# Optimization experiments

Hardware: AMD Instinct MI355X
Metric: run time of the kernel (lower is better)

Reference implementation:

```python
import jax, jax.numpy as jnp
import numpy as np

R, S, C, HID = 8192, 128, 32, 64   # rays, samples/ray, grid_chn, mlp_hidden_chn
G = 128                            # voxel grid resolution
COLOR_CHN = 3
NUM_HARM = 3
OPACITY_INIT_BIAS = -5.0
GAIN = 1.0
HE_DIM = 3 * 2 * NUM_HARM + 3      # harmonic embedding dim = 21

def _relu(x):
    return jnp.maximum(x, 0.0)

def _trilinear(grid, p):
    # grid: [G, G, G, Cg] indexed [z, y, x]; p: [N, 3] xyz coords in [-1, 1]
    g = grid.shape[0]
    c = (p + 1.0) * 0.5 * (g - 1)  # align_corners=True convention
    c0f = jnp.floor(c)
    fr = c - c0f
    c0 = jnp.clip(c0f.astype(jnp.int32), 0, g - 1)
    c1 = jnp.clip(c0 + 1, 0, g - 1)
    x0, y0, z0 = c0[:, 0], c0[:, 1], c0[:, 2]
    x1, y1, z1 = c1[:, 0], c1[:, 1], c1[:, 2]
    fx, fy, fz = fr[:, 0:1], fr[:, 1:2], fr[:, 2:3]
    out = jnp.zeros((p.shape[0], grid.shape[-1]), grid.dtype)
    for xi, wx in ((x0, 1.0 - fx), (x1, fx)):
        for yi, wy in ((y0, 1.0 - fy), (y1, fy)):
            for zi, wz in ((z0, 1.0 - fz), (z1, fz)):
                out = out + (wx * wy * wz) * grid[zi, yi, xi]
    return out

def _harmonic(d):
    # [sin(2^i d), cos(2^i d)] for i<NUM_HARM, with raw direction appended
    freqs = 2.0 ** jnp.arange(NUM_HARM, dtype=jnp.float32)
    ang = d[:, None, :] * freqs[None, :, None]  # [R, NH, 3]
    n = d.shape[0]
    return jnp.concatenate([jnp.sin(ang).reshape(n, -1), jnp.cos(ang).reshape(n, -1), d], axis=-1)

def _forward(origins, directions, near, far, feature_grid, Wr, br, Wt1, bt1, Wt2, bt2, Wo1, bo1, Wo2, bo2, Wc1, bc1, Wc2, bc2):
    n_rays = origins.shape[0]
    # stratified midpoints between near and far
    t = near[:, None] + (far - near)[:, None] * (jnp.arange(S, dtype=jnp.float32) + 0.5) / S
    pts = origins[:, None, :] + t[..., None] * directions[:, None, :]  # [R, S, 3]
    feats = _trilinear(feature_grid, pts.reshape(-1, 3)).reshape(n_rays, S, -1)
    # trunk MLP
    e = _relu(feats @ Wt1 + bt1)
    e = _relu(e @ Wt2 + bt2)
    # opacity MLP (last-layer bias carries opacity_init_bias)
    raw = _relu(e @ Wo1 + bo1) @ Wo2 + bo2  # [R, S, 1]
    density = jax.nn.softplus(GAIN * raw[..., 0])
    delta = ((far - near) / S)[:, None]
    alpha = 1.0 - jnp.exp(-delta * density)  # [R, S]
    trans = jnp.cumprod(1.0 - alpha, axis=1)
    T = jnp.concatenate([jnp.ones((n_rays, 1), alpha.dtype), trans[:, :-1]], axis=1)
    w = T * alpha  # compositing weights
    # color branch: harmonic ray-direction encoding added to color-MLP input
    ray_enc = _harmonic(directions) @ Wr + br  # [R, HID]
    cin = e + ray_enc[:, None, :]
    col = jax.nn.sigmoid(_relu(cin @ Wc1 + bc1) @ Wc2 + bc2)  # [R, S, COLOR_CHN]
    color = jnp.einsum('rs,rsc->rc', w, col)
    mask = 1.0 - trans[:, -1]
    color = color + (1.0 - mask)[:, None] * 0.0  # bg_color = 0.0
    return color, mask

def setup_inputs():
    key = jax.random.key(0)
    ks = jax.random.split(key, 16)
    directions = jax.random.normal(ks[0], (R, 3), jnp.float32)
    directions = directions / jnp.linalg.norm(directions, axis=-1, keepdims=True)
    origins = jnp.zeros((R, 3), jnp.float32)
    near = jnp.full((R,), 0.1, jnp.float32)
    far = jnp.full((R,), 1.0, jnp.float32)
    feature_grid = jax.random.normal(ks[1], (G, G, G, C), jnp.float32) * 0.1
    def lin(k, i, o):
        s = (2.0 / (i + o)) ** 0.5
        return jax.random.normal(k, (i, o), jnp.float32) * s
    return {
        'origins': origins, 'directions': directions, 'near': near, 'far': far,
        'feature_grid': feature_grid,
        'Wr': lin(ks[2], HE_DIM, HID), 'br': jnp.zeros((HID,), jnp.float32),
        'Wt1': lin(ks[3], C, HID), 'bt1': jnp.zeros((HID,), jnp.float32),
        'Wt2': lin(ks[4], HID, HID), 'bt2': jnp.zeros((HID,), jnp.float32),
        'Wo1': lin(ks[5], HID, HID), 'bo1': jnp.zeros((HID,), jnp.float32),
        'Wo2': lin(ks[6], HID, 1), 'bo2': jnp.full((1,), OPACITY_INIT_BIAS, jnp.float32),
        'Wc1': lin(ks[7], HID, HID), 'bc1': jnp.zeros((HID,), jnp.float32),
        'Wc2': lin(ks[8], HID, COLOR_CHN), 'bc2': jnp.zeros((COLOR_CHN,), jnp.float32),
    }

def reference(origins, directions, near, far, feature_grid, Wr, br, Wt1, bt1, Wt2, bt2, Wo1, bo1, Wo2, bo2, Wc1, bc1, Wc2, bc2):
    return _forward(origins, directions, near, far, feature_grid, Wr, br, Wt1, bt1, Wt2, bt2, Wo1, bo1, Wo2, bo2, Wc1, bc1, Wc2, bc2)
```

## Files before the change

### kernel.cpp

```cpp
#include <hip/hip_runtime.h>
#include <math.h>

#define NRAYS 8192
#define XPAD 72

typedef short s16x8 __attribute__((ext_vector_type(8)));
typedef float f32x4 __attribute__((ext_vector_type(4)));

__device__ __forceinline__ unsigned short f2bf(float x){
  unsigned u = __float_as_uint(x);
  u += 0x7FFF + ((u >> 16) & 1);
  return (unsigned short)(u >> 16);
}
__device__ __forceinline__ float bf2f(unsigned short s){ return __uint_as_float(((unsigned)s) << 16); }
__device__ __forceinline__ float softplusf_(float x){ return (x > 20.f) ? x : log1pf(expf(x)); }
__device__ __forceinline__ float sigmoidf_(float x){ return 1.f / (1.f + expf(-x)); }

__global__ void prep_weights(const float* __restrict__ Wt1, const float* __restrict__ Wt2,
                             const float* __restrict__ Wo1, const float* __restrict__ Wc1,
                             unsigned short* __restrict__ ws)
{
  const int i0 = blockIdx.x * blockDim.x + threadIdx.x;
  const int st = gridDim.x * blockDim.x;
  for (int i = i0; i < 2048; i += st){ int n = i >> 5, k = i & 31; ws[i]         = f2bf(Wt1[k * 64 + n]); }
  for (int i = i0; i < 4096; i += st){ int n = i >> 6, k = i & 63; ws[2048 + i]  = f2bf(Wt2[k * 64 + n]); }
  for (int i = i0; i < 4096; i += st){ int n = i >> 6, k = i & 63; ws[6144 + i]  = f2bf(Wo1[k * 64 + n]); }
  for (int i = i0; i < 4096; i += st){ int n = i >> 6, k = i & 63; ws[10240 + i] = f2bf(Wc1[k * 64 + n]); }
}

__device__ __forceinline__ void layer64(const s16x8 a[4][2], const unsigned short* __restrict__ wt,
                                        const float* __restrict__ bias, int ln15, int quad,
                                        f32x4 acc[4][4])
{
  float bv[4];
#pragma unroll
  for (int nt = 0; nt < 4; ++nt) bv[nt] = bias[nt * 16 + ln15];
#pragma unroll
  for (int mt = 0; mt < 4; ++mt)
#pragma unroll
    for (int nt = 0; nt < 4; ++nt){ f32x4 c; c[0] = bv[nt]; c[1] = bv[nt]; c[2] = bv[nt]; c[3] = bv[nt]; acc[mt][nt] = c; }
#pragma unroll
  for (int ks = 0; ks < 2; ++ks){
    s16x8 b[4];
#pragma unroll
    for (int nt = 0; nt < 4; ++nt)
      b[nt] = *(const s16x8*)(wt + (nt * 16 + ln15) * 64 + ks * 32 + quad * 8);
#pragma unroll
    for (int mt = 0; mt < 4; ++mt)
#pragma unroll
      for (int nt = 0; nt < 4; ++nt)
        acc[mt][nt] = __builtin_amdgcn_mfma_f32_16x16x32_bf16(a[mt][ks], b[nt], acc[mt][nt], 0, 0, 0);
  }
}

__device__ __forceinline__ void store_relu(unsigned short* __restrict__ sX, int wrow, int ln15, int quad,
                                           const f32x4 acc[4][4])
{
#pragma unroll
  for (int mt = 0; mt < 4; ++mt){
    const int rowb = wrow + mt * 16 + quad * 4;
#pragma unroll
    for (int nt = 0; nt < 4; ++nt){
      const int col = nt * 16 + ln15;
#pragma unroll
      for (int r = 0; r < 4; ++r)
        sX[(rowb + r) * XPAD + col] = f2bf(fmaxf(acc[mt][nt][r], 0.f));
    }
  }
}

extern "C" __global__ __launch_bounds__(256, 2)
void lightplane_fwd(const float* __restrict__ origins, const float* __restrict__ dirs,
                    const float* __restrict__ nearv,   const float* __restrict__ farv,
                    const float* __restrict__ grid,
                    const float* __restrict__ Wr,  const float* __restrict__ br,
                    const float* __restrict__ bt1, const float* __restrict__ bt2,
                    const float* __restrict__ bo1,
                    const float* __restrict__ Wo2, const float* __restrict__ bo2,
                    const float* __restrict__ bc1,
                    const float* __restrict__ Wc2, const float* __restrict__ bc2,
                    const unsigned short* __restrict__ ws,
                    float* __restrict__ out)
{
  __shared__ unsigned short s_X[256 * XPAD];
  __shared__ float s_scan[2][128];
  __shared__ float s_enc[2][64];
  __shared__ float s_part[2][2][4];

  const int tid   = threadIdx.x;
  const int lane  = tid & 63;
  const int wv    = tid >> 6;
  const int ln15  = lane & 15, quad = lane >> 4;
  const int wrow  = wv * 64;
  const int r_loc = tid >> 7;
  const int s_idx = tid & 127;
  const int ray   = blockIdx.x * 2 + r_loc;

  if (tid < 128) {
    const int rr = tid >> 6, j = tid & 63;
    const int rg = blockIdx.x * 2 + rr;
    const float ddx = dirs[rg * 3 + 0], ddy = dirs[rg * 3 + 1], ddz = dirs[rg * 3 + 2];
    float h[21]; float f = 1.f;
#pragma unroll
    for (int q = 0; q < 3; ++q) {
      h[q * 3 + 0] = sinf(ddx * f); h[q * 3 + 1] = sinf(ddy * f); h[q * 3 + 2] = sinf(ddz * f);
      h[9 + q * 3 + 0] = cosf(ddx * f); h[9 + q * 3 + 1] = cosf(ddy * f); h[9 + q * 3 + 2] = cosf(ddz * f);
      f *= 2.f;
    }
    h[18] = ddx; h[19] = ddy; h[20] = ddz;
    float a = br[j];
#pragma unroll
    for (int i = 0; i < 21; ++i) a = fmaf(h[i], Wr[i * 64 + j], a);
    s_enc[rr][j] = a;
  }

  const float dx = dirs[ray * 3 + 0], dy = dirs[ray * 3 + 1], dz = dirs[ray * 3 + 2];
  const float ox = origins[ray * 3 + 0], oy = origins[ray * 3 + 1], oz = origins[ray * 3 + 2];
  const float nr = nearv[ray], fa = farv[ray];
  const float t  = nr + (fa - nr) * ((s_idx + 0.5f) * (1.0f / 128.0f));
  const float px = fmaf(t, dx, ox), py = fmaf(t, dy, oy), pz = fmaf(t, dz, oz);

  const float cx = (px + 1.f) * 63.5f, cy = (py + 1.f) * 63.5f, cz = (pz + 1.f) * 63.5f;
  const float fx0 = floorf(cx), fy0 = floorf(cy), fz0 = floorf(cz);
  const float frx = cx - fx0, fry = cy - fy0, frz = cz - fz0;
  int ix0 = min(max((int)fx0, 0), 127), iy0 = min(max((int)fy0, 0), 127), iz0 = min(max((int)fz0, 0), 127);
  int ix1 = min(ix0 + 1, 127), iy1 = min(iy0 + 1, 127), iz1 = min(iz0 + 1, 127);
  const float wxs[2] = {1.f - frx, frx}, wys[2] = {1.f - fry, fry}, wzs[2] = {1.f - frz, frz};
  const int xi[2] = {ix0, ix1}, yi[2] = {iy0, iy1}, zi[2] = {iz0, iz1};

  float fe[32];
#pragma unroll
  for (int k = 0; k < 32; ++k) fe[k] = 0.f;
#pragma unroll
  for (int a = 0; a < 2; ++a)
#pragma unroll
    for (int b2 = 0; b2 < 2; ++b2)
#pragma unroll
      for (int c2 = 0; c2 < 2; ++c2) {
        const float wgt = wzs[a] * wys[b2] * wxs[c2];
        const float4* g4 = (const float4*)(grid + ((size_t)((zi[a] * 128 + yi[b2]) * 128 + xi[c2])) * 32);
#pragma unroll
        for (int k = 0; k < 8; ++k) {
          float4 g = g4[k];
          fe[4 * k + 0] = fmaf(wgt, g.x, fe[4 * k + 0]);
          fe[4 * k + 1] = fmaf(wgt, g.y, fe[4 * k + 1]);
          fe[4 * k + 2] = fmaf(wgt, g.z, fe[4 * k + 2]);
          fe[4 * k + 3] = fmaf(wgt, g.w, fe[4 * k + 3]);
        }
      }

#pragma unroll
  for (int q = 0; q < 4; ++q) {
    s16x8 v;
#pragma unroll
    for (int j = 0; j < 8; ++j) v[j] = (short)f2bf(fe[q * 8 + j]);
    *(s16x8*)&s_X[tid * XPAD + q * 8] = v;
  }

  f32x4 acc[4][4];

  {
    s16x8 a1[4];
#pragma unroll
    for (int mt = 0; mt < 4; ++mt)
      a1[mt] = *(const s16x8*)&s_X[(wrow + mt * 16 + ln15) * XPAD + quad * 8];
    float bv[4];
#pragma unroll
    for (int nt = 0; nt < 4; ++nt) bv[nt] = bt1[nt * 16 + ln15];
#pragma unroll
    for (int mt = 0; mt < 4; ++mt)
#pragma unroll
      for (int nt = 0; nt < 4; ++nt){ f32x4 c; c[0]=bv[nt];c[1]=bv[nt];c[2]=bv[nt];c[3]=bv[nt]; acc[mt][nt]=c; }
    s16x8 b[4];
#pragma unroll
    for (int nt = 0; nt < 4; ++nt)
      b[nt] = *(const s16x8*)(ws + (nt * 16 + ln15) * 32 + quad * 8);
#pragma unroll
    for (int mt = 0; mt < 4; ++mt)
#pragma unroll
      for (int nt = 0; nt < 4; ++nt)
        acc[mt][nt] = __builtin_amdgcn_mfma_f32_16x16x32_bf16(a1[mt], b[nt], acc[mt][nt], 0, 0, 0);
    store_relu(s_X, wrow, ln15, quad, acc);
  }

  {
    s16x8 a[4][2];
#pragma unroll
    for (int ks = 0; ks < 2; ++ks)
#pragma unroll
      for (int mt = 0; mt < 4; ++mt)
        a[mt][ks] = *(const s16x8*)&s_X[(wrow + mt * 16 + ln15) * XPAD + ks * 32 + quad * 8];
    layer64(a, ws + 2048, bt2, ln15, quad, acc);
    store_relu(s_X, wrow, ln15, quad, acc);
  }

  s16x8 ea[4][2];
#pragma unroll
  for (int ks = 0; ks < 2; ++ks)
#pragma unroll
    for (int mt = 0; mt < 4; ++mt)
      ea[mt][ks] = *(const s16x8*)&s_X[(wrow + mt * 16 + ln15) * XPAD + ks * 32 + quad * 8];

  layer64(ea, ws + 6144, bo1, ln15, quad, acc);
  store_relu(s_X, wrow, ln15, quad, acc);
  float raw = bo2[0];
#pragma unroll
  for (int q = 0; q < 8; ++q) {
    s16x8 v = *(const s16x8*)&s_X[tid * XPAD + q * 8];
#pragma unroll
    for (int j = 0; j < 8; ++j)
      raw = fmaf(bf2f((unsigned short)v[j]), Wo2[q * 8 + j], raw);
  }
  const float density = softplusf_(raw);
  const float delta   = (fa - nr) * (1.0f / 128.0f);
  const float alpha   = 1.f - expf(-delta * density);

  __syncthreads();

  {
    s16x8 a[4][2];
#pragma unroll
    for (int ks = 0; ks < 2; ++ks) {
      const float* ep = &s_enc[r_loc][ks * 32 + quad * 8];
      float4 e0 = *(const float4*)ep;
      float4 e1 = *(const float4*)(ep + 4);
      float encv[8] = {e0.x, e0.y, e0.z, e0.w, e1.x, e1.y, e1.z, e1.w};
#pragma unroll
      for (int mt = 0; mt < 4; ++mt) {
        s16x8 v;
#pragma unroll
        for (int j = 0; j < 8; ++j)
          v[j] = (short)f2bf(bf2f((unsigned short)ea[mt][ks][j]) + encv[j]);
        a[mt][ks] = v;
      }
    }
    layer64(a, ws + 10240, bc1, ln15, quad, acc);
    store_relu(s_X, wrow, ln15, quad, acc);
  }
  float c0 = bc2[0], c1 = bc2[1], c2 = bc2[2];
#pragma unroll
  for (int q = 0; q < 8; ++q) {
    s16x8 v = *(const s16x8*)&s_X[tid * XPAD + q * 8];
#pragma unroll
    for (int j = 0; j < 8; ++j) {
      const float h = bf2f((unsigned short)v[j]);
      c0 = fmaf(h, Wc2[(q * 8 + j) * 3 + 0], c0);
      c1 = fmaf(h, Wc2[(q * 8 + j) * 3 + 1], c1);
      c2 = fmaf(h, Wc2[(q * 8 + j) * 3 + 2], c2);
    }
  }
  c0 = sigmoidf_(c0); c1 = sigmoidf_(c1); c2 = sigmoidf_(c2);

  float vv = 1.f - alpha;
  s_scan[r_loc][s_idx] = vv;
  __syncthreads();
#pragma unroll
  for (int off = 1; off < 128; off <<= 1) {
    const float u = (s_idx >= off) ? s_scan[r_loc][s_idx - off] : 1.f;
    __syncthreads();
    vv *= u;
    s_scan[r_loc][s_idx] = vv;
    __syncthreads();
  }
  const float Texcl = (s_idx == 0) ? 1.f : s_scan[r_loc][s_idx - 1];
  const float wgt = Texcl * alpha;

  float p0 = wgt * c0, p1 = wgt * c1, p2 = wgt * c2;
#pragma unroll
  for (int off = 32; off > 0; off >>= 1) {
    p0 += __shfl_down(p0, off, 64);
    p1 += __shfl_down(p1, off, 64);
    p2 += __shfl_down(p2, off, 64);
  }
  if ((tid & 63) == 0) {
    const int wvi = s_idx >> 6;
    s_part[r_loc][wvi][0] = p0; s_part[r_loc][wvi][1] = p1; s_part[r_loc][wvi][2] = p2;
  }
  __syncthreads();
  if (s_idx == 0) {
    out[ray * 3 + 0] = s_part[r_loc][0][0] + s_part[r_loc][1][0];
    out[ray * 3 + 1] = s_part[r_loc][0][1] + s_part[r_loc][1][1];
    out[ray * 3 + 2] = s_part[r_loc][0][2] + s_part[r_loc][1][2];
    out[NRAYS * 3 + ray] = 1.f - s_scan[r_loc][127];
  }
}

extern "C" void kernel_launch(void* const* d_in, const int* in_sizes, int n_in,
                              void* d_out, int out_size, void* d_ws, size_t ws_size,
                              hipStream_t stream)
{
  (void)in_sizes; (void)n_in; (void)out_size; (void)ws_size;
  const float* origins = (const float*)d_in[0];
  const float* dirs    = (const float*)d_in[1];
  const float* nearv   = (const float*)d_in[2];
  const float* farv    = (const float*)d_in[3];
  const float* grid    = (const float*)d_in[4];
  const float* Wr  = (const float*)d_in[5];
  const float* br  = (const float*)d_in[6];
  const float* Wt1 = (const float*)d_in[7];
  const float* bt1 = (const float*)d_in[8];
  const float* Wt2 = (const float*)d_in[9];
  const float* bt2 = (const float*)d_in[10];
  const float* Wo1 = (const float*)d_in[11];
  const float* bo1 = (const float*)d_in[12];
  const float* Wo2 = (const float*)d_in[13];
  const float* bo2 = (const float*)d_in[14];
  const float* Wc1 = (const float*)d_in[15];
  const float* bc1 = (const float*)d_in[16];
  const float* Wc2 = (const float*)d_in[17];
  const float* bc2 = (const float*)d_in[18];
  unsigned short* ws = (unsigned short*)d_ws;
  float* out = (float*)d_out;

  prep_weights<<<16, 256, 0, stream>>>(Wt1, Wt2, Wo1, Wc1, ws);
  lightplane_fwd<<<NRAYS / 2, 256, 0, stream>>>(origins, dirs, nearv, farv, grid,
                                                Wr, br, bt1, bt2, bo1, Wo2, bo2,
                                                bc1, Wc2, bc2, ws, out);
}
```

Before: 509.4 us.

## Raise occupancy, restructure trilinear gather, and use wavefront shuffle scan

Raises the launch-bounds occupancy hint from 2 to 4 blocks per SM. The trilinear gather now loads 16-byte chunks from all 8 corners together and accumulates them in short per-chunk registers, so the 32-float accumulator array is gone and register pressure drops. The direction encoding moves after the gather. The 128-element shared-memory transmittance scan with about 14 barriers becomes an intra-wavefront shuffle scan plus one cross-wave combine. Forcing 4 blocks per SM may cause register spills, and the scan's multiplication order changes, which can shift floating-point results slightly.

```diff
diff --git a/kernel.cpp b/kernel.cpp
--- a/kernel.cpp
+++ b/kernel.cpp
@@ -69,7 +69,7 @@
   }
 }
 
-extern "C" __global__ __launch_bounds__(256, 2)
+extern "C" __global__ __launch_bounds__(256, 4)
 void lightplane_fwd(const float* __restrict__ origins, const float* __restrict__ dirs,
                     const float* __restrict__ nearv,   const float* __restrict__ farv,
                     const float* __restrict__ grid,
@@ -83,9 +83,9 @@
                     float* __restrict__ out)
 {
   __shared__ unsigned short s_X[256 * XPAD];
-  __shared__ float s_scan[2][128];
   __shared__ float s_enc[2][64];
   __shared__ float s_part[2][2][4];
+  __shared__ float s_wtot[4];
 
   const int tid   = threadIdx.x;
   const int lane  = tid & 63;
@@ -96,24 +96,6 @@
   const int s_idx = tid & 127;
   const int ray   = blockIdx.x * 2 + r_loc;
 
-  if (tid < 128) {
-    const int rr = tid >> 6, j = tid & 63;
-    const int rg = blockIdx.x * 2 + rr;
-    const float ddx = dirs[rg * 3 + 0], ddy = dirs[rg * 3 + 1], ddz = dirs[rg * 3 + 2];
-    float h[21]; float f = 1.f;
-#pragma unroll
-    for (int q = 0; q < 3; ++q) {
-      h[q * 3 + 0] = sinf(ddx * f); h[q * 3 + 1] = sinf(ddy * f); h[q * 3 + 2] = sinf(ddz * f);
-      h[9 + q * 3 + 0] = cosf(ddx * f); h[9 + q * 3 + 1] = cosf(ddy * f); h[9 + q * 3 + 2] = cosf(ddz * f);
-      f *= 2.f;
-    }
-    h[18] = ddx; h[19] = ddy; h[20] = ddz;
-    float a = br[j];
-#pragma unroll
-    for (int i = 0; i < 21; ++i) a = fmaf(h[i], Wr[i * 64 + j], a);
-    s_enc[rr][j] = a;
-  }
-
   const float dx = dirs[ray * 3 + 0], dy = dirs[ray * 3 + 1], dz = dirs[ray * 3 + 2];
   const float ox = origins[ray * 3 + 0], oy = origins[ray * 3 + 1], oz = origins[ray * 3 + 2];
   const float nr = nearv[ray], fa = farv[ray];
@@ -128,33 +110,62 @@
   const float wxs[2] = {1.f - frx, frx}, wys[2] = {1.f - fry, fry}, wzs[2] = {1.f - frz, frz};
   const int xi[2] = {ix0, ix1}, yi[2] = {iy0, iy1}, zi[2] = {iz0, iz1};
 
-  float fe[32];
-#pragma unroll
-  for (int k = 0; k < 32; ++k) fe[k] = 0.f;
-#pragma unroll
-  for (int a = 0; a < 2; ++a)
-#pragma unroll
-    for (int b2 = 0; b2 < 2; ++b2)
-#pragma unroll
-      for (int c2 = 0; c2 < 2; ++c2) {
-        const float wgt = wzs[a] * wys[b2] * wxs[c2];
-        const float4* g4 = (const float4*)(grid + ((size_t)((zi[a] * 128 + yi[b2]) * 128 + xi[c2])) * 32);
-#pragma unroll
-        for (int k = 0; k < 8; ++k) {
-          float4 g = g4[k];
-          fe[4 * k + 0] = fmaf(wgt, g.x, fe[4 * k + 0]);
-          fe[4 * k + 1] = fmaf(wgt, g.y, fe[4 * k + 1]);
-          fe[4 * k + 2] = fmaf(wgt, g.z, fe[4 * k + 2]);
-          fe[4 * k + 3] = fmaf(wgt, g.w, fe[4 * k + 3]);
-        }
+  int  coff[8];
+  float cw[8];
+#pragma unroll
+  for (int zz = 0; zz < 2; ++zz)
+#pragma unroll
+    for (int yy = 0; yy < 2; ++yy)
+#pragma unroll
+      for (int xx = 0; xx < 2; ++xx) {
+        const int c = zz * 4 + yy * 2 + xx;
+        coff[c] = ((zi[zz] * 128 + yi[yy]) * 128 + xi[xx]) * 128;
+        cw[c]   = wzs[zz] * wys[yy] * wxs[xx];
       }
-
-#pragma unroll
-  for (int q = 0; q < 4; ++q) {
-    s16x8 v;
-#pragma unroll
-    for (int j = 0; j < 8; ++j) v[j] = (short)f2bf(fe[q * 8 + j]);
-    *(s16x8*)&s_X[tid * XPAD + q * 8] = v;
+  const char* __restrict__ gbase = (const char*)grid;
+
+#pragma unroll
+  for (int qp = 0; qp < 4; ++qp) {
+    s16x8 pk;
+#pragma unroll
+    for (int h = 0; h < 2; ++h) {
+      const int q = qp * 2 + h;
+      float4 v[8];
+#pragma unroll
+      for (int c = 0; c < 8; ++c)
+        v[c] = *(const float4*)(gbase + coff[c] + q * 16);
+      float f0 = 0.f, f1 = 0.f, f2 = 0.f, f3 = 0.f;
+#pragma unroll
+      for (int c = 0; c < 8; ++c) {
+        f0 = fmaf(cw[c], v[c].x, f0);
+        f1 = fmaf(cw[c], v[c].y, f1);
+        f2 = fmaf(cw[c], v[c].z, f2);
+        f3 = fmaf(cw[c], v[c].w, f3);
+      }
+      pk[h * 4 + 0] = (short)f2bf(f0);
+      pk[h * 4 + 1] = (short)f2bf(f1);
+      pk[h * 4 + 2] = (short)f2bf(f2);
+      pk[h * 4 + 3] = (short)f2bf(f3);
+    }
+    *(s16x8*)&s_X[tid * XPAD + qp * 8] = pk;
+  }
+
+  if (tid < 128) {
+    const int rr = tid >> 6, j = tid & 63;
+    const int rg = blockIdx.x * 2 + rr;
+    const float ddx = dirs[rg * 3 + 0], ddy = dirs[rg * 3 + 1], ddz = dirs[rg * 3 + 2];
+    float h[21]; float f = 1.f;
+#pragma unroll
+    for (int q = 0; q < 3; ++q) {
+      h[q * 3 + 0] = sinf(ddx * f); h[q * 3 + 1] = sinf(ddy * f); h[q * 3 + 2] = sinf(ddz * f);
+      h[9 + q * 3 + 0] = cosf(ddx * f); h[9 + q * 3 + 1] = cosf(ddy * f); h[9 + q * 3 + 2] = cosf(ddz * f);
+      f *= 2.f;
+    }
+    h[18] = ddx; h[19] = ddy; h[20] = ddz;
+    float a = br[j];
+#pragma unroll
+    for (int i = 0; i < 21; ++i) a = fmaf(h[i], Wr[i * 64 + j], a);
+    s_enc[rr][j] = a;
   }
 
   f32x4 acc[4][4];
@@ -251,19 +262,19 @@
   }
   c0 = sigmoidf_(c0); c1 = sigmoidf_(c1); c2 = sigmoidf_(c2);
 
-  float vv = 1.f - alpha;
-  s_scan[r_loc][s_idx] = vv;
+  float sc = 1.f - alpha;
+#pragma unroll
+  for (int off = 1; off < 64; off <<= 1) {
+    const float u = __shfl_up(sc, off, 64);
+    if (lane >= off) sc *= u;
+  }
+  float excl = __shfl_up(sc, 1, 64);
+  if (lane == 0) excl = 1.f;
+  if (lane == 63) s_wtot[wv] = sc;
   __syncthreads();
-#pragma unroll
-  for (int off = 1; off < 128; off <<= 1) {
-    const float u = (s_idx >= off) ? s_scan[r_loc][s_idx - off] : 1.f;
-    __syncthreads();
-    vv *= u;
-    s_scan[r_loc][s_idx] = vv;
-    __syncthreads();
-  }
-  const float Texcl = (s_idx == 0) ? 1.f : s_scan[r_loc][s_idx - 1];
-  const float wgt = Texcl * alpha;
+  const int w_in_ray = s_idx >> 6;
+  const float prefix = w_in_ray ? s_wtot[r_loc * 2] : 1.f;
+  const float wgt = prefix * excl * alpha;
 
   float p0 = wgt * c0, p1 = wgt * c1, p2 = wgt * c2;
 #pragma unroll
@@ -272,16 +283,15 @@
     p1 += __shfl_down(p1, off, 64);
     p2 += __shfl_down(p2, off, 64);
   }
-  if ((tid & 63) == 0) {
-    const int wvi = s_idx >> 6;
-    s_part[r_loc][wvi][0] = p0; s_part[r_loc][wvi][1] = p1; s_part[r_loc][wvi][2] = p2;
+  if (lane == 0) {
+    s_part[r_loc][w_in_ray][0] = p0; s_part[r_loc][w_in_ray][1] = p1; s_part[r_loc][w_in_ray][2] = p2;
   }
   __syncthreads();
   if (s_idx == 0) {
     out[ray * 3 + 0] = s_part[r_loc][0][0] + s_part[r_loc][1][0];
     out[ray * 3 + 1] = s_part[r_loc][0][1] + s_part[r_loc][1][1];
     out[ray * 3 + 2] = s_part[r_loc][0][2] + s_part[r_loc][1][2];
-    out[NRAYS * 3 + ray] = 1.f - s_scan[r_loc][127];
+    out[NRAYS * 3 + ray] = 1.f - s_wtot[r_loc * 2] * s_wtot[r_loc * 2 + 1];
   }
 }
 
```

Measured after the change: 563.0 us. +10.5%, slower.
